# Kernel optimization log

Measured on AMD Instinct MI355X. Metric: run time of the kernel, lower is better.

## Reference

```python
import jax, jax.numpy as jnp
import numpy as np

DIM = 128
LAYERS = 3
N_NODES = 50000
N_EDGES = 640000
LN_EPS = 1e-5


def setup_inputs() -> dict:
    key = jax.random.key(0)
    ks = jax.random.split(key, 10)
    s = 1.0 / np.sqrt(DIM)
    x = jax.random.normal(ks[0], (N_NODES, DIM), dtype=jnp.float32)
    edge_index = jax.random.randint(ks[1], (2, N_EDGES), 0, N_NODES, dtype=jnp.int64)
    in_w = jax.random.uniform(ks[2], (DIM, DIM), jnp.float32, -s, s)
    in_b = jax.random.uniform(ks[3], (DIM,), jnp.float32, -s, s)
    w1 = jax.random.uniform(ks[4], (LAYERS, DIM, DIM), jnp.float32, -s, s)
    b1 = jax.random.uniform(ks[5], (LAYERS, DIM), jnp.float32, -s, s)
    w2 = jax.random.uniform(ks[6], (LAYERS, DIM, DIM), jnp.float32, -s, s)
    b2 = jax.random.uniform(ks[7], (LAYERS, DIM), jnp.float32, -s, s)
    ln_g = jnp.ones((LAYERS, DIM), jnp.float32)
    ln_b = jnp.zeros((LAYERS, DIM), jnp.float32)
    return {"x": x, "edge_index": edge_index, "in_w": in_w, "in_b": in_b,
            "w1": w1, "b1": b1, "w2": w2, "b2": b2, "ln_g": ln_g, "ln_b": ln_b}


def _layer_norm(z, g, b):
    mu = jnp.mean(z, axis=-1, keepdims=True)
    var = jnp.mean(jnp.square(z - mu), axis=-1, keepdims=True)
    return (z - mu) * jax.lax.rsqrt(var + LN_EPS) * g + b


def reference(x, edge_index, in_w, in_b, w1, b1, w2, b2, ln_g, ln_b):
    src, dst = edge_index[0], edge_index[1]
    n = x.shape[0]
    # degree is identical every layer in the original; compute once (same math)
    deg = jax.ops.segment_sum(jnp.ones(dst.shape, x.dtype), dst, num_segments=n)
    deg = jnp.maximum(deg, 1.0)[:, None]  # [N,1]
    h = x @ in_w + in_b  # [N,D]
    for i in range(w1.shape[0]):
        m = jax.ops.segment_sum(h[src], dst, num_segments=n) / deg  # gather+scatter
        mlp = jax.nn.relu(m @ w1[i] + b1[i]) @ w2[i] + b2[i]
        h = _layer_norm(h + mlp, ln_g[i], ln_b[i])
    return h
```

## Files before the change

kernel.cpp:

```cpp
#include <hip/hip_runtime.h>
#include <hip/hip_fp8.h>

#define DIM 128
#define LN_EPS 1e-5f

typedef __attribute__((ext_vector_type(8))) short s16x8;
typedef __attribute__((ext_vector_type(4))) float f32x4;
typedef __attribute__((ext_vector_type(2))) float f32x2;
typedef __attribute__((ext_vector_type(4))) unsigned int u32x4;
typedef __attribute__((ext_vector_type(2))) unsigned int u32x2;

__device__ __forceinline__ unsigned short f2bf(float f) {
    unsigned u = __float_as_uint(f);
    unsigned r = u + 0x7fffu + ((u >> 16) & 1u);
    return (unsigned short)(r >> 16);
}
__device__ __forceinline__ float bf2f(unsigned short b) {
    return __uint_as_float(((unsigned)b) << 16);
}
__device__ __forceinline__ unsigned char f2fp8(float f) {
    return (unsigned char)__hip_cvt_float_to_fp8(f, __HIP_SATFINITE, __HIP_E4M3);
}
__device__ __forceinline__ void acc_fp8x4(float* a, unsigned v) {
    f32x2 lo = __builtin_amdgcn_cvt_pk_f32_fp8(v, false);
    f32x2 hi = __builtin_amdgcn_cvt_pk_f32_fp8(v, true);
    a[0] += lo[0]; a[1] += lo[1]; a[2] += hi[0]; a[3] += hi[1];
}


__global__ void count_deg(const int* __restrict__ dst, int E, int* __restrict__ counts) {
    int i = blockIdx.x * 256 + threadIdx.x;
    if (i < E) atomicAdd(&counts[dst[i]], 1);
}

__global__ __launch_bounds__(256) void scan_partials(const int* __restrict__ counts, int n,
                                                     int* __restrict__ bsum) {
    int base = blockIdx.x * 1024 + threadIdx.x * 4;
    int s = 0;
#pragma unroll
    for (int j = 0; j < 4; ++j) {
        int i = base + j;
        if (i < n) s += counts[i];
    }
#pragma unroll
    for (int off = 32; off > 0; off >>= 1) s += __shfl_xor(s, off, 64);
    __shared__ int wsum[4];
    int lane = threadIdx.x & 63, wid = threadIdx.x >> 6;
    if (lane == 0) wsum[wid] = s;
    __syncthreads();
    if (threadIdx.x == 0) bsum[blockIdx.x] = wsum[0] + wsum[1] + wsum[2] + wsum[3];
}

__global__ __launch_bounds__(64) void scan_bsums(const int* __restrict__ bsum,
                                                 int* __restrict__ bofs, int nb,
                                                 int* __restrict__ rowptr, int N, int E) {
    int lane = threadIdx.x;
    int carry = 0;
    for (int base = 0; base < nb; base += 64) {
        int v = (base + lane < nb) ? bsum[base + lane] : 0;
        int incl = v;
#pragma unroll
        for (int off = 1; off < 64; off <<= 1) {
            int t = __shfl_up(incl, off, 64);
            if (lane >= off) incl += t;
        }
        if (base + lane < nb) bofs[base + lane] = carry + incl - v;
        carry += __shfl(incl, 63, 64);
    }
    if (lane == 0) rowptr[N] = E;
}

__global__ __launch_bounds__(256) void scan_final(const int* __restrict__ counts, int n,
                                                  const int* __restrict__ bofs,
                                                  int* __restrict__ rowptr,
                                                  int* __restrict__ cursor,
                                                  float* __restrict__ dinv) {
    int base = blockIdx.x * 1024 + threadIdx.x * 4;
    int v[4];
#pragma unroll
    for (int j = 0; j < 4; ++j) {
        int i = base + j;
        v[j] = (i < n) ? counts[i] : 0;
    }
    int tsum = v[0] + v[1] + v[2] + v[3];
    int lane = threadIdx.x & 63, wid = threadIdx.x >> 6;
    int incl = tsum;
#pragma unroll
    for (int off = 1; off < 64; off <<= 1) {
        int t = __shfl_up(incl, off, 64);
        if (lane >= off) incl += t;
    }
    __shared__ int wsum[4];
    if (lane == 63) wsum[wid] = incl;
    __syncthreads();
    int wofs = 0;
    for (int w = 0; w < 4; ++w)
        if (w < wid) wofs += wsum[w];
    int excl = bofs[blockIdx.x] + wofs + (incl - tsum);
#pragma unroll
    for (int j = 0; j < 4; ++j) {
        int i = base + j;
        if (i < n) {
            rowptr[i] = excl;
            cursor[i] = excl;
            dinv[i] = 1.0f / (float)((v[j] > 1) ? v[j] : 1);
            excl += v[j];
        }
    }
}

__global__ void fill_csr(const int* __restrict__ src, const int* __restrict__ dst, int E,
                         int* __restrict__ cursor, int* __restrict__ srcidx) {
    int i = blockIdx.x * 256 + threadIdx.x;
    if (i < E) {
        int p = atomicAdd(&cursor[dst[i]], 1);
        srcidx[p] = src[i];
    }
}


__global__ __launch_bounds__(256) void cvt_weights(const float* __restrict__ in_w,
                                                   const float* __restrict__ w1,
                                                   const float* __restrict__ w2,
                                                   unsigned short* __restrict__ wt, int L) {
    int mat = blockIdx.x >> 3, part = blockIdx.x & 7;
    const float* src;
    if (mat == 0) src = in_w;
    else if (mat <= L) src = w1 + (size_t)(mat - 1) * DIM * DIM;
    else src = w2 + (size_t)(mat - 1 - L) * DIM * DIM;
    unsigned short* dst = wt + (size_t)mat * DIM * DIM;
    int base = part * 2048 + threadIdx.x;
#pragma unroll
    for (int j = 0; j < 8; ++j) {
        int i = base + j * 256;
        int k = i >> 7, n = i & 127;
        dst[n * DIM + k] = f2bf(src[i]);
    }
}


__global__ __launch_bounds__(256) void gemm_bias_mfma(const float* __restrict__ x,
                                                      const unsigned short* __restrict__ Wt,
                                                      const float* __restrict__ bias,
                                                      unsigned short* __restrict__ hb,
                                                      unsigned char* __restrict__ h8, int N) {
    int tid = threadIdx.x;
    int s = tid >> 6, lane = tid & 63;
    int quad = lane >> 4, l16 = lane & 15;
    int r0 = blockIdx.x * 16;
    int cs = s * 32;
    int arow = r0 + l16;
    bool av = arow < N;

    f32x4 acc[2];
    acc[0] = (f32x4){0.f, 0.f, 0.f, 0.f};
    acc[1] = (f32x4){0.f, 0.f, 0.f, 0.f};

    const float4* xp = (const float4*)(x + ((size_t)(av ? arow : 0) << 7)) + quad * 2;
#pragma unroll
    for (int k0 = 0; k0 < 128; k0 += 32) {
        s16x8 a = {0, 0, 0, 0, 0, 0, 0, 0};
        if (av) {
            float4 f0 = xp[k0 / 4];
            float4 f1 = xp[k0 / 4 + 1];
            a[0] = (short)f2bf(f0.x); a[1] = (short)f2bf(f0.y);
            a[2] = (short)f2bf(f0.z); a[3] = (short)f2bf(f0.w);
            a[4] = (short)f2bf(f1.x); a[5] = (short)f2bf(f1.y);
            a[6] = (short)f2bf(f1.z); a[7] = (short)f2bf(f1.w);
        }
        s16x8 b0 = *(const s16x8*)(Wt + ((size_t)(cs + l16) << 7) + quad * 8 + k0);
        s16x8 b1 = *(const s16x8*)(Wt + ((size_t)(cs + 16 + l16) << 7) + quad * 8 + k0);
        acc[0] = __builtin_amdgcn_mfma_f32_16x16x32_bf16(a, b0, acc[0], 0, 0, 0);
        acc[1] = __builtin_amdgcn_mfma_f32_16x16x32_bf16(a, b1, acc[1], 0, 0, 0);
    }

#pragma unroll
    for (int c = 0; c < 2; ++c) {
        int col = cs + c * 16 + l16;
        float bv = bias[col];
#pragma unroll
        for (int reg = 0; reg < 4; ++reg) {
            int grow = r0 + quad * 4 + reg;
            if (grow < N) {
                float o = acc[c][reg] + bv;
                hb[((size_t)grow << 7) + col] = f2bf(o);
                h8[((size_t)grow << 7) + col] = f2fp8(o);
            }
        }
    }
}


__global__ __launch_bounds__(256) void agg_mlp_ln(const unsigned short* __restrict__ hin,
                                                  const unsigned char* __restrict__ h8in,
                                                  const int* __restrict__ rowptr,
                                                  const int* __restrict__ srcidx,
                                                  const float* __restrict__ dinv,
                                                  const unsigned short* __restrict__ W1t,
                                                  const float* __restrict__ B1,
                                                  const unsigned short* __restrict__ W2t,
                                                  const float* __restrict__ B2,
                                                  const float* __restrict__ G,
                                                  const float* __restrict__ Bb,
                                                  unsigned short* __restrict__ hout,
                                                  unsigned char* __restrict__ h8out,
                                                  float* __restrict__ out_f32, int N) {
    __shared__ unsigned short M[16][132];
    __shared__ unsigned short P[16][132];
    __shared__ float s1p[4][16], s2p[4][16];

    int tid = threadIdx.x;
    int s = tid >> 6, lane = tid & 63;
    int quad = lane >> 4, l16 = lane & 15;
    int g = lane >> 2, li = lane & 3;
    int r0 = blockIdx.x * 16;
    int cs = s * 32;

    int nd = r0 + g;
    bool nv = nd < N;
    int e  = nv ? rowptr[nd] : 0;
    int ee = nv ? rowptr[nd + 1] : 0;

    float a0[8] = {0, 0, 0, 0, 0, 0, 0, 0};
    float a1[8] = {0, 0, 0, 0, 0, 0, 0, 0};
    const unsigned char* hsl = h8in + cs + li * 8;

    while (__any(e < ee)) {
        int myidx = (e + li < ee) ? srcidx[e + li] : 0;
        int i0 = __shfl(myidx, (g << 2) | 0, 64);
        int i1 = __shfl(myidx, (g << 2) | 1, 64);
        int i2 = __shfl(myidx, (g << 2) | 2, 64);
        int i3 = __shfl(myidx, (g << 2) | 3, 64);
        bool p0 = e < ee, p1 = e + 1 < ee, p2 = e + 2 < ee, p3 = e + 3 < ee;
        u32x2 v0, v1, v2, v3;
        if (p0) v0 = *(const u32x2*)(hsl + ((size_t)i0 << 7));
        if (p1) v1 = *(const u32x2*)(hsl + ((size_t)i1 << 7));
        if (p2) v2 = *(const u32x2*)(hsl + ((size_t)i2 << 7));
        if (p3) v3 = *(const u32x2*)(hsl + ((size_t)i3 << 7));
        if (p0) { acc_fp8x4(a0,     v0[0]); acc_fp8x4(a0 + 4, v0[1]); }
        if (p1) { acc_fp8x4(a1,     v1[0]); acc_fp8x4(a1 + 4, v1[1]); }
        if (p2) { acc_fp8x4(a0,     v2[0]); acc_fp8x4(a0 + 4, v2[1]); }
        if (p3) { acc_fp8x4(a1,     v3[0]); acc_fp8x4(a1 + 4, v3[1]); }
        e += 4;
    }

    {
        float di = nv ? dinv[nd] : 0.f;
        u32x4 o;
#pragma unroll
        for (int j = 0; j < 4; ++j) {
            unsigned lo = f2bf((a0[2 * j]     + a1[2 * j])     * di);
            unsigned hi = f2bf((a0[2 * j + 1] + a1[2 * j + 1]) * di);
            o[j] = lo | (hi << 16);
        }
        *(u32x4*)(&M[g][cs + li * 8]) = o;
    }
    __syncthreads();

    f32x4 acc[2];
    acc[0] = (f32x4){0.f, 0.f, 0.f, 0.f};
    acc[1] = (f32x4){0.f, 0.f, 0.f, 0.f};
#pragma unroll
    for (int k0 = 0; k0 < 128; k0 += 32) {
        s16x8 a = *(const s16x8*)(&M[l16][quad * 8 + k0]);
        s16x8 b0 = *(const s16x8*)(W1t + ((size_t)(cs + l16) << 7) + quad * 8 + k0);
        s16x8 b1 = *(const s16x8*)(W1t + ((size_t)(cs + 16 + l16) << 7) + quad * 8 + k0);
        acc[0] = __builtin_amdgcn_mfma_f32_16x16x32_bf16(a, b0, acc[0], 0, 0, 0);
        acc[1] = __builtin_amdgcn_mfma_f32_16x16x32_bf16(a, b1, acc[1], 0, 0, 0);
    }
#pragma unroll
    for (int c = 0; c < 2; ++c) {
        int col = cs + c * 16 + l16;
        float bv = B1[col];
#pragma unroll
        for (int reg = 0; reg < 4; ++reg) {
            float v = fmaxf(acc[c][reg] + bv, 0.f);
            P[quad * 4 + reg][col] = f2bf(v);
        }
    }
    __syncthreads();

    acc[0] = (f32x4){0.f, 0.f, 0.f, 0.f};
    acc[1] = (f32x4){0.f, 0.f, 0.f, 0.f};
#pragma unroll
    for (int k0 = 0; k0 < 128; k0 += 32) {
        s16x8 a = *(const s16x8*)(&P[l16][quad * 8 + k0]);
        s16x8 b0 = *(const s16x8*)(W2t + ((size_t)(cs + l16) << 7) + quad * 8 + k0);
        s16x8 b1 = *(const s16x8*)(W2t + ((size_t)(cs + 16 + l16) << 7) + quad * 8 + k0);
        acc[0] = __builtin_amdgcn_mfma_f32_16x16x32_bf16(a, b0, acc[0], 0, 0, 0);
        acc[1] = __builtin_amdgcn_mfma_f32_16x16x32_bf16(a, b1, acc[1], 0, 0, 0);
    }

    float z[2][4];
    float ps1[4] = {0, 0, 0, 0}, ps2[4] = {0, 0, 0, 0};
#pragma unroll
    for (int c = 0; c < 2; ++c) {
        int col = cs + c * 16 + l16;
        float b2v = B2[col];
#pragma unroll
        for (int reg = 0; reg < 4; ++reg) {
            int grow = r0 + quad * 4 + reg;
            float hv = (grow < N) ? bf2f(hin[((size_t)grow << 7) + col]) : 0.f;
            float zz = acc[c][reg] + b2v + hv;
            z[c][reg] = zz;
            ps1[reg] += zz;
            ps2[reg] += zz * zz;
        }
    }
#pragma unroll
    for (int off = 1; off < 16; off <<= 1) {
#pragma unroll
        for (int reg = 0; reg < 4; ++reg) {
            ps1[reg] += __shfl_xor(ps1[reg], off, 64);
            ps2[reg] += __shfl_xor(ps2[reg], off, 64);
        }
    }
    if (l16 == 0) {
#pragma unroll
        for (int reg = 0; reg < 4; ++reg) {
            s1p[s][quad * 4 + reg] = ps1[reg];
            s2p[s][quad * 4 + reg] = ps2[reg];
        }
    }
    __syncthreads();

#pragma unroll
    for (int reg = 0; reg < 4; ++reg) {
        int row = quad * 4 + reg;
        float S1 = s1p[0][row] + s1p[1][row] + s1p[2][row] + s1p[3][row];
        float S2 = s2p[0][row] + s2p[1][row] + s2p[2][row] + s2p[3][row];
        float mean = S1 * (1.0f / 128.0f);
        float var = S2 * (1.0f / 128.0f) - mean * mean;
        float rs = rsqrtf(var + LN_EPS);
        int grow = r0 + row;
        if (grow < N) {
#pragma unroll
            for (int c = 0; c < 2; ++c) {
                int col = cs + c * 16 + l16;
                float o = (z[c][reg] - mean) * rs * G[col] + Bb[col];
                if (out_f32) {
                    out_f32[((size_t)grow << 7) + col] = o;
                } else {
                    hout[((size_t)grow << 7) + col] = f2bf(o);
                    h8out[((size_t)grow << 7) + col] = f2fp8(o);
                }
            }
        }
    }
}


extern "C" void kernel_launch(void* const* d_in, const int* in_sizes, int n_in,
                              void* d_out, int out_size, void* d_ws, size_t ws_size,
                              hipStream_t stream) {
    const float* x    = (const float*)d_in[0];
    const int*   ei   = (const int*)d_in[1];
    const float* in_w = (const float*)d_in[2];
    const float* in_b = (const float*)d_in[3];
    const float* w1   = (const float*)d_in[4];
    const float* b1   = (const float*)d_in[5];
    const float* w2   = (const float*)d_in[6];
    const float* b2   = (const float*)d_in[7];
    const float* ln_g = (const float*)d_in[8];
    const float* ln_b = (const float*)d_in[9];

    const int N = in_sizes[0] / DIM;
    const int E = in_sizes[1] / 2;
    const int LAYERS = in_sizes[4] / (DIM * DIM);

    const int* e_src = ei;
    const int* e_dst = ei + E;

    char* ws = (char*)d_ws;
    unsigned short* hb0    = (unsigned short*)ws;  ws += (size_t)N * DIM * 2;
    unsigned short* hb1    = (unsigned short*)ws;  ws += (size_t)N * DIM * 2;
    unsigned char*  h8a    = (unsigned char*)ws;   ws += (size_t)N * DIM;
    unsigned char*  h8b    = (unsigned char*)ws;   ws += (size_t)N * DIM;
    int*            counts = (int*)ws;             ws += (size_t)N * 4;
    int*            rowptr = (int*)ws;             ws += (size_t)(N + 1) * 4;
    int*            cursor = (int*)ws;             ws += (size_t)N * 4;
    float*          dinv   = (float*)ws;           ws += (size_t)N * 4;
    int*            srcidx = (int*)ws;             ws += (size_t)E * 4;
    int*            bsum   = (int*)ws;             ws += 4096;
    int*            bofs   = (int*)ws;             ws += 4096;
    unsigned short* wt     = (unsigned short*)ws;  ws += (size_t)(2 * LAYERS + 1) * DIM * DIM * 2;

    const int nScanBlocks = (N + 1023) / 1024;
    const int nMat = 2 * LAYERS + 1;

    (void)hipMemsetAsync(counts, 0, (size_t)N * 4, stream);
    count_deg<<<(E + 255) / 256, 256, 0, stream>>>(e_dst, E, counts);
    scan_partials<<<nScanBlocks, 256, 0, stream>>>(counts, N, bsum);
    scan_bsums<<<1, 64, 0, stream>>>(bsum, bofs, nScanBlocks, rowptr, N, E);
    scan_final<<<nScanBlocks, 256, 0, stream>>>(counts, N, bofs, rowptr, cursor, dinv);
    fill_csr<<<(E + 255) / 256, 256, 0, stream>>>(e_src, e_dst, E, cursor, srcidx);
    cvt_weights<<<nMat * 8, 256, 0, stream>>>(in_w, w1, w2, wt, LAYERS);

    const unsigned short* in_wt = wt;
    const unsigned short* w1t   = wt + (size_t)DIM * DIM;
    const unsigned short* w2t   = wt + (size_t)(1 + LAYERS) * DIM * DIM;

    int tile_grid = (N + 15) / 16;
    gemm_bias_mfma<<<tile_grid, 256, 0, stream>>>(x, in_wt, in_b, hb0, h8a, N);

    unsigned short* hin  = hb0;  unsigned char* h8in  = h8a;
    unsigned short* hout = hb1;  unsigned char* h8out = h8b;
    for (int i = 0; i < LAYERS; ++i) {
        float* out = (i == LAYERS - 1) ? (float*)d_out : nullptr;
        agg_mlp_ln<<<tile_grid, 256, 0, stream>>>(hin, h8in, rowptr, srcidx, dinv,
                                                  w1t + (size_t)i * DIM * DIM, b1 + (size_t)i * DIM,
                                                  w2t + (size_t)i * DIM * DIM, b2 + (size_t)i * DIM,
                                                  ln_g + (size_t)i * DIM, ln_b + (size_t)i * DIM,
                                                  hout, h8out, out, N);
        unsigned short* t = hin; hin = hout; hout = t;
        unsigned char* t8 = h8in; h8in = h8out; h8out = t8;
    }
}
```

Measured before the change: 347.8 us.

## Restructure fp8 gather to edge-per-lane with software-pipelined prefetch and shuffle reduction

The neighbor gather now gives each of the 4 lanes in a group its own edge. Each lane loads a full 32-byte slice of that source row instead of 8 bytes from four rows. Loads for the next edge batch and the index fetch for the one after are issued before accumulating the current batch, so gather latency overlaps the fp8 conversion work. A two-step xor-shuffle transpose-reduction then combines the per-lane partial sums. This costs 32 accumulator registers per lane plus extra shuffles, which may lower occupancy.

```diff
diff --git a/kernel.cpp b/kernel.cpp
--- a/kernel.cpp
+++ b/kernel.cpp
@@ -221,27 +221,58 @@
     int e  = nv ? rowptr[nd] : 0;
     int ee = nv ? rowptr[nd + 1] : 0;
 
-    float a0[8] = {0, 0, 0, 0, 0, 0, 0, 0};
-    float a1[8] = {0, 0, 0, 0, 0, 0, 0, 0};
-    const unsigned char* hsl = h8in + cs + li * 8;
-
-    while (__any(e < ee)) {
-        int myidx = (e + li < ee) ? srcidx[e + li] : 0;
-        int i0 = __shfl(myidx, (g << 2) | 0, 64);
-        int i1 = __shfl(myidx, (g << 2) | 1, 64);
-        int i2 = __shfl(myidx, (g << 2) | 2, 64);
-        int i3 = __shfl(myidx, (g << 2) | 3, 64);
-        bool p0 = e < ee, p1 = e + 1 < ee, p2 = e + 2 < ee, p3 = e + 3 < ee;
-        u32x2 v0, v1, v2, v3;
-        if (p0) v0 = *(const u32x2*)(hsl + ((size_t)i0 << 7));
-        if (p1) v1 = *(const u32x2*)(hsl + ((size_t)i1 << 7));
-        if (p2) v2 = *(const u32x2*)(hsl + ((size_t)i2 << 7));
-        if (p3) v3 = *(const u32x2*)(hsl + ((size_t)i3 << 7));
-        if (p0) { acc_fp8x4(a0,     v0[0]); acc_fp8x4(a0 + 4, v0[1]); }
-        if (p1) { acc_fp8x4(a1,     v1[0]); acc_fp8x4(a1 + 4, v1[1]); }
-        if (p2) { acc_fp8x4(a0,     v2[0]); acc_fp8x4(a0 + 4, v2[1]); }
-        if (p3) { acc_fp8x4(a1,     v3[0]); acc_fp8x4(a1 + 4, v3[1]); }
-        e += 4;
+    const unsigned char* bse = h8in + cs;
+
+    float pa[32];
+#pragma unroll
+    for (int j = 0; j < 32; ++j) pa[j] = 0.f;
+
+    bool pA = (e + li) < ee;
+    int idxA = pA ? srcidx[e + li] : 0;
+    u32x4 A0 = {0, 0, 0, 0}, A1 = {0, 0, 0, 0};
+    if (pA) {
+        const u32x4* rp = (const u32x4*)(bse + ((size_t)idxA << 7));
+        A0 = rp[0];
+        A1 = rp[1];
+    }
+    int eB = e + 4;
+    bool pB = (eB + li) < ee;
+    int idxB = pB ? srcidx[eB + li] : 0;
+
+    while (__any(pA)) {
+        u32x4 B0 = {0, 0, 0, 0}, B1v = {0, 0, 0, 0};
+        if (pB) {
+            const u32x4* rp = (const u32x4*)(bse + ((size_t)idxB << 7));
+            B0 = rp[0];
+            B1v = rp[1];
+        }
+        int eC = eB + 4;
+        bool pC = (eC + li) < ee;
+        int idxC = pC ? srcidx[eC + li] : 0;
+        acc_fp8x4(pa + 0,  A0[0]); acc_fp8x4(pa + 4,  A0[1]);
+        acc_fp8x4(pa + 8,  A0[2]); acc_fp8x4(pa + 12, A0[3]);
+        acc_fp8x4(pa + 16, A1[0]); acc_fp8x4(pa + 20, A1[1]);
+        acc_fp8x4(pa + 24, A1[2]); acc_fp8x4(pa + 28, A1[3]);
+        pA = pB; A0 = B0; A1 = B1v;
+        pB = pC; idxB = idxC; eB = eC;
+    }
+
+    float q[16];
+#pragma unroll
+    for (int j = 0; j < 8; ++j) {
+        float t0 = pa[j]      + __shfl_xor(pa[j], 1, 64);
+        float t1 = pa[j + 8]  + __shfl_xor(pa[j + 8], 1, 64);
+        float t2 = pa[j + 16] + __shfl_xor(pa[j + 16], 1, 64);
+        float t3 = pa[j + 24] + __shfl_xor(pa[j + 24], 1, 64);
+        q[j]     = (li & 1) ? t1 : t0;
+        q[j + 8] = (li & 1) ? t3 : t2;
+    }
+    float r[8];
+#pragma unroll
+    for (int j = 0; j < 8; ++j) {
+        float u0 = q[j]     + __shfl_xor(q[j], 2, 64);
+        float u1 = q[j + 8] + __shfl_xor(q[j + 8], 2, 64);
+        r[j] = (li & 2) ? u1 : u0;
     }
 
     {
@@ -249,8 +280,8 @@
         u32x4 o;
 #pragma unroll
         for (int j = 0; j < 4; ++j) {
-            unsigned lo = f2bf((a0[2 * j]     + a1[2 * j])     * di);
-            unsigned hi = f2bf((a0[2 * j + 1] + a1[2 * j + 1]) * di);
+            unsigned lo = f2bf(r[2 * j]     * di);
+            unsigned hi = f2bf(r[2 * j + 1] * di);
             o[j] = lo | (hi << 16);
         }
         *(u32x4*)(&M[g][cs + li * 8]) = o;
```

New measurement: 369.6 us. +6.3%, slower.

## Stage edge indices in LDS and software-pipeline the fp8 neighbor gather

Applied to the files above, without the earlier changes.

Each block now loads its 16 nodes' row pointers and up to 512 source indices into shared memory, then reads indices from LDS. Previously each 4-edge step did a global index load plus shuffles. The gather loop is double-buffered: the next group of row loads is issued before the current group is accumulated, so more memory requests are in flight. The residual h values are also loaded before the MLP matmuls to hide their latency. The costs are extra shared memory, two more block barriers and more registers, which may lower occupancy.

```diff
diff --git a/kernel.cpp b/kernel.cpp
--- a/kernel.cpp
+++ b/kernel.cpp
@@ -3,6 +3,7 @@
 
 #define DIM 128
 #define LN_EPS 1e-5f
+#define ECAP 512
 
 typedef __attribute__((ext_vector_type(8))) short s16x8;
 typedef __attribute__((ext_vector_type(4))) float f32x4;
@@ -208,6 +209,8 @@
     __shared__ unsigned short M[16][132];
     __shared__ unsigned short P[16][132];
     __shared__ float s1p[4][16], s2p[4][16];
+    __shared__ int eL[ECAP];
+    __shared__ int rp[17];
 
     int tid = threadIdx.x;
     int s = tid >> 6, lane = tid & 63;
@@ -216,36 +219,59 @@
     int r0 = blockIdx.x * 16;
     int cs = s * 32;
 
+    if (tid < 17) {
+        int idx = r0 + tid;
+        rp[tid] = rowptr[idx < N ? idx : N];
+    }
+    __syncthreads();
+    int ebase = rp[0];
+    int etot = rp[16] - ebase;
+    int estg = etot < ECAP ? etot : ECAP;
+    for (int i = tid; i < estg; i += 256) eL[i] = srcidx[ebase + i];
+    __syncthreads();
+
     int nd = r0 + g;
     bool nv = nd < N;
-    int e  = nv ? rowptr[nd] : 0;
-    int ee = nv ? rowptr[nd + 1] : 0;
+    int ls = rp[g] - ebase;
+    int le = rp[g + 1] - ebase;
+    if (!nv) { ls = 0; le = 0; }
+    float di = nv ? dinv[nd] : 0.f;
+
+    const unsigned char* hsl = h8in + cs + li * 8;
 
     float a0[8] = {0, 0, 0, 0, 0, 0, 0, 0};
     float a1[8] = {0, 0, 0, 0, 0, 0, 0, 0};
-    const unsigned char* hsl = h8in + cs + li * 8;
-
-    while (__any(e < ee)) {
-        int myidx = (e + li < ee) ? srcidx[e + li] : 0;
-        int i0 = __shfl(myidx, (g << 2) | 0, 64);
-        int i1 = __shfl(myidx, (g << 2) | 1, 64);
-        int i2 = __shfl(myidx, (g << 2) | 2, 64);
-        int i3 = __shfl(myidx, (g << 2) | 3, 64);
-        bool p0 = e < ee, p1 = e + 1 < ee, p2 = e + 2 < ee, p3 = e + 3 < ee;
-        u32x2 v0, v1, v2, v3;
-        if (p0) v0 = *(const u32x2*)(hsl + ((size_t)i0 << 7));
-        if (p1) v1 = *(const u32x2*)(hsl + ((size_t)i1 << 7));
-        if (p2) v2 = *(const u32x2*)(hsl + ((size_t)i2 << 7));
-        if (p3) v3 = *(const u32x2*)(hsl + ((size_t)i3 << 7));
-        if (p0) { acc_fp8x4(a0,     v0[0]); acc_fp8x4(a0 + 4, v0[1]); }
-        if (p1) { acc_fp8x4(a1,     v1[0]); acc_fp8x4(a1 + 4, v1[1]); }
-        if (p2) { acc_fp8x4(a0,     v2[0]); acc_fp8x4(a0 + 4, v2[1]); }
-        if (p3) { acc_fp8x4(a1,     v3[0]); acc_fp8x4(a1 + 4, v3[1]); }
-        e += 4;
-    }
+
+#define LIDX(jj) (((jj) < le) ? (((jj) < ECAP) ? eL[(jj)] : srcidx[ebase + (jj)]) : -1)
+
+    int jA = ls;
+    int iA0 = LIDX(jA + 0), iA1 = LIDX(jA + 1), iA2 = LIDX(jA + 2), iA3 = LIDX(jA + 3);
+    u32x2 A0 = {0, 0}, A1 = {0, 0}, A2 = {0, 0}, A3 = {0, 0};
+    if (iA0 >= 0) A0 = *(const u32x2*)(hsl + ((size_t)iA0 << 7));
+    if (iA1 >= 0) A1 = *(const u32x2*)(hsl + ((size_t)iA1 << 7));
+    if (iA2 >= 0) A2 = *(const u32x2*)(hsl + ((size_t)iA2 << 7));
+    if (iA3 >= 0) A3 = *(const u32x2*)(hsl + ((size_t)iA3 << 7));
+    int jB = jA + 4;
+    int iB0 = LIDX(jB + 0), iB1 = LIDX(jB + 1), iB2 = LIDX(jB + 2), iB3 = LIDX(jB + 3);
+
+    while (__any(jA < le)) {
+        u32x2 B0 = {0, 0}, B1v = {0, 0}, B2v = {0, 0}, B3 = {0, 0};
+        if (iB0 >= 0) B0  = *(const u32x2*)(hsl + ((size_t)iB0 << 7));
+        if (iB1 >= 0) B1v = *(const u32x2*)(hsl + ((size_t)iB1 << 7));
+        if (iB2 >= 0) B2v = *(const u32x2*)(hsl + ((size_t)iB2 << 7));
+        if (iB3 >= 0) B3  = *(const u32x2*)(hsl + ((size_t)iB3 << 7));
+        int jC = jB + 4;
+        int iC0 = LIDX(jC + 0), iC1 = LIDX(jC + 1), iC2 = LIDX(jC + 2), iC3 = LIDX(jC + 3);
+        acc_fp8x4(a0, A0[0]); acc_fp8x4(a0 + 4, A0[1]);
+        acc_fp8x4(a1, A1[0]); acc_fp8x4(a1 + 4, A1[1]);
+        acc_fp8x4(a0, A2[0]); acc_fp8x4(a0 + 4, A2[1]);
+        acc_fp8x4(a1, A3[0]); acc_fp8x4(a1 + 4, A3[1]);
+        jA = jB; A0 = B0; A1 = B1v; A2 = B2v; A3 = B3;
+        jB = jC; iB0 = iC0; iB1 = iC1; iB2 = iC2; iB3 = iC3;
+    }
+#undef LIDX
 
     {
-        float di = nv ? dinv[nd] : 0.f;
         u32x4 o;
 #pragma unroll
         for (int j = 0; j < 4; ++j) {
@@ -256,6 +282,17 @@
         *(u32x4*)(&M[g][cs + li * 8]) = o;
     }
     __syncthreads();
+
+    unsigned short hvr[2][4];
+#pragma unroll
+    for (int c = 0; c < 2; ++c) {
+        int col = cs + c * 16 + l16;
+#pragma unroll
+        for (int reg = 0; reg < 4; ++reg) {
+            int grow = r0 + quad * 4 + reg;
+            hvr[c][reg] = (grow < N) ? hin[((size_t)grow << 7) + col] : (unsigned short)0;
+        }
+    }
 
     f32x4 acc[2];
     acc[0] = (f32x4){0.f, 0.f, 0.f, 0.f};
@@ -299,8 +336,7 @@
         float b2v = B2[col];
 #pragma unroll
         for (int reg = 0; reg < 4; ++reg) {
-            int grow = r0 + quad * 4 + reg;
-            float hv = (grow < N) ? bf2f(hin[((size_t)grow << 7) + col]) : 0.f;
+            float hv = bf2f(hvr[c][reg]);
             float zz = acc[c][reg] + b2v + hv;
             z[c][reg] = zz;
             ps1[reg] += zz;
```

New measurement: 353.8 us. About the same (+1.7%).
